# Optimization experiments

Hardware: AMD Instinct MI355X
Metric: run time of the kernel (lower is better)

## Reference

```python
import jax, jax.numpy as jnp
import numpy as np

N = 100000      # nodes
E = 3200000     # edges
G = 1024        # graphs in the batch
D_IN = 128      # input feature dim
H = 64          # hidden dim
BN_EPS = 1e-5


def _linear_init(key, fan_in, shape):
    bound = 1.0 / np.sqrt(fan_in)
    return jax.random.uniform(key, shape, jnp.float32, -bound, bound)


def setup_inputs() -> dict:
    key = jax.random.key(0)
    ks = jax.random.split(key, 16)
    x = jax.random.normal(ks[0], (N, D_IN), jnp.float32)
    edge_index = jax.random.randint(ks[1], (2, E), 0, N, dtype=jnp.int32)
    batch = jnp.sort(jax.random.randint(ks[2], (N,), 0, G, dtype=jnp.int32))
    inp = {"x": x, "edge_index": edge_index, "batch": batch}
    # layer 0 MLP: Linear(D_IN,H) -> ReLU -> BN(H) -> Linear(H,H) -> ReLU
    inp["W1_0"] = _linear_init(ks[3], D_IN, (D_IN, H))
    inp["b1_0"] = _linear_init(ks[4], D_IN, (H,))
    inp["g_0"] = jnp.ones((H,), jnp.float32)
    inp["be_0"] = jnp.zeros((H,), jnp.float32)
    inp["W2_0"] = _linear_init(ks[5], H, (H, H))
    inp["b2_0"] = _linear_init(ks[6], H, (H,))
    # layer 1 MLP: Linear(H,H) -> ReLU -> BN(H) -> Linear(H,H) -> ReLU
    inp["W1_1"] = _linear_init(ks[7], H, (H, H))
    inp["b1_1"] = _linear_init(ks[8], H, (H,))
    inp["g_1"] = jnp.ones((H,), jnp.float32)
    inp["be_1"] = jnp.zeros((H,), jnp.float32)
    inp["W2_1"] = _linear_init(ks[9], H, (H, H))
    inp["b2_1"] = _linear_init(ks[10], H, (H,))
    return inp


def _mlp(h, W1, b1, g, be, W2, b2):
    h = jnp.maximum(h @ W1 + b1, 0.0)
    mu = h.mean(axis=0)                      # BatchNorm1d (training: batch stats)
    var = h.var(axis=0)                      # biased variance, as torch normalizes
    h = g * (h - mu) * jax.lax.rsqrt(var + BN_EPS) + be
    return jnp.maximum(h @ W2 + b2, 0.0)


def _gin(h, src, dst, mlp_params):
    # GINConv, eps=0: out = mlp(x_i + sum_{j->i} x_j)
    agg = jax.ops.segment_sum(h[src], dst, num_segments=N)
    return _mlp(h + agg, *mlp_params)


def reference(x, edge_index, batch,
              W1_0, b1_0, g_0, be_0, W2_0, b2_0,
              W1_1, b1_1, g_1, be_1, W2_1, b2_1):
    src, dst = edge_index[0], edge_index[1]
    h = _gin(x, src, dst, (W1_0, b1_0, g_0, be_0, W2_0, b2_0))
    h = _gin(h, src, dst, (W1_1, b1_1, g_1, be_1, W2_1, b2_1))
    x_g = jax.ops.segment_sum(h, batch, num_segments=G)  # global add pooling
    return (x_g, h)
```

## Files before the change

### kernel.cpp

```cpp
#include <hip/hip_runtime.h>

static inline int cdiv_ll(long long a, long long b){ return (int)((a + b - 1) / b); }

#define EB_CHUNK 8192
#define NPB 256
#define MAXNB 512
#define CSR_LDS 10240

typedef short bf16x8 __attribute__((ext_vector_type(8)));
typedef float f32x4 __attribute__((ext_vector_type(4)));

__device__ __forceinline__ float bf2f(unsigned short h) {
  unsigned u = (unsigned)h << 16;
  return __uint_as_float(u);
}
__device__ __forceinline__ unsigned short f2bf(float f) {
  unsigned u = __float_as_uint(f);
  u += 0x7FFF + ((u >> 16) & 1);
  return (unsigned short)(u >> 16);
}

#define SWZ(row, byteoff) ((byteoff) ^ (((row) & 7) << 4))

template<int K, bool RELU>
__device__ __forceinline__ void stage_x_bf16(
    char* XlB, const float* __restrict__ X, long long rb, int M)
{
  for (int f = threadIdx.x; f < 16 * K; f += 256) {
    int r = f / (K / 4), c4 = (f % (K / 4)) * 4;
    float4 v = make_float4(0.f, 0.f, 0.f, 0.f);
    if (rb + r < M) {
      v = *reinterpret_cast<const float4*>(X + (rb + r) * K + c4);
      if (RELU) {
        v.x = fmaxf(v.x, 0.f); v.y = fmaxf(v.y, 0.f);
        v.z = fmaxf(v.z, 0.f); v.w = fmaxf(v.w, 0.f);
      }
    }
    ushort4 h; h.x = f2bf(v.x); h.y = f2bf(v.y); h.z = f2bf(v.z); h.w = f2bf(v.w);
    *reinterpret_cast<ushort4*>(XlB + r * (2 * K) + SWZ(r, c4 * 2)) = h;
  }
}

template<int K>
__device__ __forceinline__ void stage_wt_bf16(char* WTB, const float* __restrict__ W)
{
  for (int t = threadIdx.x; t < K * 32; t += 256) {
    int c = t & 63, kp = t >> 6;
    float w0 = W[(2 * kp) * 64 + c];
    float w1 = W[(2 * kp + 1) * 64 + c];
    ushort2 hh; hh.x = f2bf(w0); hh.y = f2bf(w1);
    *reinterpret_cast<ushort2*>(WTB + c * (2 * K) + SWZ(c, 4 * kp)) = hh;
  }
}

template<int K>
__device__ __forceinline__ void mfma_chain(
    f32x4* acc, const char* XlB, const char* WTB, int wv, int lr, int lg)
{
  const int rowb = 16 * wv + lr;
  #pragma unroll
  for (int kc = 0; kc < K / 32; ++kc) {
    const int kByte = kc * 64 + lg * 16;
    bf16x8 a = *reinterpret_cast<const bf16x8*>(XlB + rowb * (2 * K) + SWZ(rowb, kByte));
    #pragma unroll
    for (int ct = 0; ct < 4; ++ct) {
      int c = ct * 16 + lr;
      bf16x8 b = *reinterpret_cast<const bf16x8*>(WTB + c * (2 * K) + SWZ(c, kByte));
      acc[ct] = __builtin_amdgcn_mfma_f32_16x16x32_bf16(a, b, acc[ct], 0, 0, 0);
    }
  }
}

template<int K, bool IN_RELU, bool RELU_OUT, bool BIAS, bool OUT_BF16>
__global__ __launch_bounds__(256) void mfma_gemm(
    const float* __restrict__ X, const float* __restrict__ W,
    const float* __restrict__ bias, void* __restrict__ Yv, int M)
{
  __shared__ __align__(16) char XlB[64 * 2 * K];
  __shared__ __align__(16) char WTB[64 * 2 * K];
  const long long rb = (long long)blockIdx.x * 64;
  stage_x_bf16<K, IN_RELU>(XlB, X, rb, M);
  stage_wt_bf16<K>(WTB, W);
  __syncthreads();

  const int lane = threadIdx.x & 63, wv = threadIdx.x >> 6;
  const int lr = lane & 15, lg = lane >> 4;
  f32x4 acc[4] = {};
  mfma_chain<K>(acc, XlB, WTB, wv, lr, lg);

  #pragma unroll
  for (int ct = 0; ct < 4; ++ct) {
    const int c = ct * 16 + lr;
    const float bv = BIAS ? bias[c] : 0.0f;
    #pragma unroll
    for (int j = 0; j < 4; ++j) {
      long long row = rb + 16 * wv + lg * 4 + j;
      if (row < M) {
        float v = acc[ct][j] + bv;
        if (RELU_OUT) v = fmaxf(v, 0.f);
        if (OUT_BF16) ((unsigned short*)Yv)[row * 64 + c] = f2bf(v);
        else          ((float*)Yv)[row * 64 + c] = v;
      }
    }
  }
}

__global__ __launch_bounds__(256) void mfma_dual(
    const float* __restrict__ A, const float* __restrict__ Wa,
    const float* __restrict__ ba, const float* __restrict__ Wb,
    unsigned short* __restrict__ P, int M)
{
  __shared__ __align__(16) char XlB[64 * 128];
  __shared__ __align__(16) char WTaB[64 * 128];
  __shared__ __align__(16) char WTbB[64 * 128];
  __shared__ __align__(16) char Xl2B[64 * 128];
  const long long rb = (long long)blockIdx.x * 64;
  stage_x_bf16<64, true>(XlB, A, rb, M);
  stage_wt_bf16<64>(WTaB, Wa);
  stage_wt_bf16<64>(WTbB, Wb);
  __syncthreads();

  const int lane = threadIdx.x & 63, wv = threadIdx.x >> 6;
  const int lr = lane & 15, lg = lane >> 4;
  f32x4 acc[4] = {};
  mfma_chain<64>(acc, XlB, WTaB, wv, lr, lg);

  #pragma unroll
  for (int ct = 0; ct < 4; ++ct) {
    const int c = ct * 16 + lr;
    const float bv = ba[c];
    #pragma unroll
    for (int j = 0; j < 4; ++j) {
      int rloc = 16 * wv + lg * 4 + j;
      float v = fmaxf(acc[ct][j] + bv, 0.f);
      *reinterpret_cast<unsigned short*>(Xl2B + rloc * 128 + SWZ(rloc, c * 2)) = f2bf(v);
    }
  }
  __syncthreads();

  f32x4 ac2[4] = {};
  mfma_chain<64>(ac2, Xl2B, WTbB, wv, lr, lg);

  #pragma unroll
  for (int ct = 0; ct < 4; ++ct) {
    const int c = ct * 16 + lr;
    #pragma unroll
    for (int j = 0; j < 4; ++j) {
      long long row = rb + 16 * wv + lg * 4 + j;
      if (row < M) P[row * 64 + c] = f2bf(ac2[ct][j]);
    }
  }
}

__global__ __launch_bounds__(256) void part_hist(
    const int* __restrict__ dst, int* __restrict__ blockHist,
    int E, int NB, int nblocksB)
{
  __shared__ int hist[MAXNB];
  for (int i = threadIdx.x; i < NB; i += 256) hist[i] = 0;
  __syncthreads();
  int base = blockIdx.x * EB_CHUNK;
  int end = min(base + EB_CHUNK, E);
  for (int e = base + threadIdx.x; e < end; e += 256)
    atomicAdd(&hist[dst[e] >> 8], 1);
  __syncthreads();
  for (int i = threadIdx.x; i < NB; i += 256)
    blockHist[(long long)i * nblocksB + blockIdx.x] = hist[i];
}

__global__ __launch_bounds__(256) void scan_bucket_blocks(
    int* __restrict__ blockHist, int* __restrict__ bucketTotal, int nblocksB)
{
  int* row = blockHist + (long long)blockIdx.x * nblocksB;
  __shared__ int tsum[256];
  int v[4]; int local = 0;
  int i0 = threadIdx.x * 4;
  #pragma unroll
  for (int k = 0; k < 4; ++k) { int g = i0 + k; v[k] = (g < nblocksB) ? row[g] : 0; local += v[k]; }
  tsum[threadIdx.x] = local;
  __syncthreads();
  for (int off = 1; off < 256; off <<= 1) {
    int y = (threadIdx.x >= off) ? tsum[threadIdx.x - off] : 0;
    __syncthreads();
    tsum[threadIdx.x] += y;
    __syncthreads();
  }
  int pref = tsum[threadIdx.x] - local;
  #pragma unroll
  for (int k = 0; k < 4; ++k) { int g = i0 + k; if (g < nblocksB) { row[g] = pref; pref += v[k]; } }
  if (threadIdx.x == 255) bucketTotal[blockIdx.x] = tsum[255];
}

__global__ __launch_bounds__(512) void scan_buckets(
    const int* __restrict__ bucketTotal, int* __restrict__ bucketBase, int NB)
{
  __shared__ int tsum[512];
  int t = threadIdx.x;
  int v = (t < NB) ? bucketTotal[t] : 0;
  tsum[t] = v;
  __syncthreads();
  for (int off = 1; off < 512; off <<= 1) {
    int y = (t >= off) ? tsum[t - off] : 0;
    __syncthreads();
    tsum[t] += y;
    __syncthreads();
  }
  if (t < NB) bucketBase[t] = tsum[t] - v;
  if (t == NB - 1) bucketBase[NB] = tsum[t];
}

__global__ __launch_bounds__(256) void part_scatter(
    const int* __restrict__ src, const int* __restrict__ dst,
    const int* __restrict__ blockHist, const int* __restrict__ bucketBase,
    unsigned* __restrict__ ebuf, int E, int NB, int nblocksB)
{
  __shared__ int cursor[MAXNB];
  for (int i = threadIdx.x; i < NB; i += 256)
    cursor[i] = bucketBase[i] + blockHist[(long long)i * nblocksB + blockIdx.x];
  __syncthreads();
  int base = blockIdx.x * EB_CHUNK;
  int end = min(base + EB_CHUNK, E);
  for (int e = base + threadIdx.x; e < end; e += 256) {
    int s = src[e], d = dst[e];
    int p = atomicAdd(&cursor[d >> 8], 1);
    ebuf[p] = (unsigned)s | ((unsigned)(d & (NPB - 1)) << 24);
  }
}

__global__ __launch_bounds__(256) void bucket_csr(
    const unsigned* __restrict__ ebuf, const int* __restrict__ bucketBase,
    int* __restrict__ rowptr, int* __restrict__ col, int N, int NB)
{
  int b = blockIdx.x;
  int eb = bucketBase[b], ee = bucketBase[b + 1];
  int cnt = ee - eb;
  int nodeBase = b * NPB;
  __shared__ unsigned ebl[CSR_LDS];
  __shared__ int hist[NPB];
  __shared__ int tsum[NPB];
  __shared__ int cur[NPB];
  const bool fit = (cnt <= CSR_LDS);
  hist[threadIdx.x] = 0;
  if (fit) for (int i = threadIdx.x; i < cnt; i += 256) ebl[i] = ebuf[eb + i];
  __syncthreads();
  for (int i = threadIdx.x; i < cnt; i += 256)
    atomicAdd(&hist[(fit ? ebl[i] : ebuf[eb + i]) >> 24], 1);
  __syncthreads();
  int local = hist[threadIdx.x];
  tsum[threadIdx.x] = local;
  __syncthreads();
  for (int off = 1; off < 256; off <<= 1) {
    int y = (threadIdx.x >= off) ? tsum[threadIdx.x - off] : 0;
    __syncthreads();
    tsum[threadIdx.x] += y;
    __syncthreads();
  }
  int pref = tsum[threadIdx.x] - local;
  int node = nodeBase + threadIdx.x;
  if (node < N) rowptr[node] = eb + pref;
  if (b == NB - 1 && threadIdx.x == 0) rowptr[N] = ee;
  cur[threadIdx.x] = pref;
  __syncthreads();
  for (int i = threadIdx.x; i < cnt; i += 256) {
    unsigned w = fit ? ebl[i] : ebuf[eb + i];
    int l = (int)(w >> 24);
    int p = eb + atomicAdd(&cur[l], 1);
    col[p] = (int)(w & 0xFFFFFFu);
  }
}

__global__ __launch_bounds__(256) void gin_gather_bf16(
    const int* __restrict__ rowptr, const int* __restrict__ col,
    const unsigned short* __restrict__ P, const float* __restrict__ b1,
    float* __restrict__ A, float* __restrict__ stats, int N, int nodeStride)
{
  const int lane = threadIdx.x & 63;
  const int wv = threadIdx.x >> 6;
  const int q = lane >> 4;
  const int cl = lane & 15;
  float s[4] = {0.f, 0.f, 0.f, 0.f};
  float sq[4] = {0.f, 0.f, 0.f, 0.f};
  const float4 bb = *reinterpret_cast<const float4*>(b1 + 4 * cl);

  for (int node = blockIdx.x * 4 + wv; node < N; node += nodeStride) {
    const int beg = rowptr[node], end = rowptr[node + 1];
    float a0 = 0.f, a1 = 0.f, a2 = 0.f, a3 = 0.f;
    if (q == 1) {
      ushort4 h = *reinterpret_cast<const ushort4*>(P + (long long)node * 64 + 4 * cl);
      a0 = bf2f(h.x); a1 = bf2f(h.y); a2 = bf2f(h.z); a3 = bf2f(h.w);
    } else if (q == 2) {
      a0 = bb.x; a1 = bb.y; a2 = bb.z; a3 = bb.w;
    }
    int j = beg + q;
    for (; j + 12 < end; j += 16) {
      int rA = col[j], rB = col[j + 4], rC = col[j + 8], rD = col[j + 12];
      ushort4 hA = *reinterpret_cast<const ushort4*>(P + (long long)rA * 64 + 4 * cl);
      ushort4 hB = *reinterpret_cast<const ushort4*>(P + (long long)rB * 64 + 4 * cl);
      ushort4 hC = *reinterpret_cast<const ushort4*>(P + (long long)rC * 64 + 4 * cl);
      ushort4 hD = *reinterpret_cast<const ushort4*>(P + (long long)rD * 64 + 4 * cl);
      a0 += bf2f(hA.x); a1 += bf2f(hA.y); a2 += bf2f(hA.z); a3 += bf2f(hA.w);
      a0 += bf2f(hB.x); a1 += bf2f(hB.y); a2 += bf2f(hB.z); a3 += bf2f(hB.w);
      a0 += bf2f(hC.x); a1 += bf2f(hC.y); a2 += bf2f(hC.z); a3 += bf2f(hC.w);
      a0 += bf2f(hD.x); a1 += bf2f(hD.y); a2 += bf2f(hD.z); a3 += bf2f(hD.w);
    }
    for (; j < end; j += 4) {
      int rA = col[j];
      ushort4 hA = *reinterpret_cast<const ushort4*>(P + (long long)rA * 64 + 4 * cl);
      a0 += bf2f(hA.x); a1 += bf2f(hA.y); a2 += bf2f(hA.z); a3 += bf2f(hA.w);
    }
    a0 += __shfl_xor(a0, 16); a0 += __shfl_xor(a0, 32);
    a1 += __shfl_xor(a1, 16); a1 += __shfl_xor(a1, 32);
    a2 += __shfl_xor(a2, 16); a2 += __shfl_xor(a2, 32);
    a3 += __shfl_xor(a3, 16); a3 += __shfl_xor(a3, 32);
    if (q == 0) {
      *reinterpret_cast<float4*>(A + (long long)node * 64 + 4 * cl) =
          make_float4(a0, a1, a2, a3);
    } else if (q == 1) {
      float r0 = fmaxf(a0, 0.f), r1 = fmaxf(a1, 0.f);
      float r2 = fmaxf(a2, 0.f), r3 = fmaxf(a3, 0.f);
      s[0] += r0; s[1] += r1; s[2] += r2; s[3] += r3;
      sq[0] += r0 * r0; sq[1] += r1 * r1; sq[2] += r2 * r2; sq[3] += r3 * r3;
    }
  }

  __shared__ float st[4][16][8];
  if (q == 1) {
    st[wv][cl][0] = s[0]; st[wv][cl][1] = s[1]; st[wv][cl][2] = s[2]; st[wv][cl][3] = s[3];
    st[wv][cl][4] = sq[0]; st[wv][cl][5] = sq[1]; st[wv][cl][6] = sq[2]; st[wv][cl][7] = sq[3];
  }
  __syncthreads();
  if (threadIdx.x < 128) {
    int c = threadIdx.x;
    int colid = c & 63, part = c >> 6;
    int idx = (part ? 4 : 0) + (colid & 3);
    float v = st[0][colid >> 2][idx] + st[1][colid >> 2][idx]
            + st[2][colid >> 2][idx] + st[3][colid >> 2][idx];
    atomicAdd(&stats[c], v);
  }
}

__global__ void bn_fold(
    const float* __restrict__ stats, const float* __restrict__ g, const float* __restrict__ be,
    const float* __restrict__ W2, const float* __restrict__ b2,
    float* __restrict__ W2f, float* __restrict__ b2f, float invN)
{
  int j = threadIdx.x;
  __shared__ float sc[64], sh[64];
  float mu = stats[j] * invN;
  float var = stats[64 + j] * invN - mu * mu;
  float s = g[j] * rsqrtf(var + 1e-5f);
  sc[j] = s;
  sh[j] = be[j] - mu * s;
  __syncthreads();
  float acc = b2[j];
  for (int k = 0; k < 64; ++k) {
    float w = W2[k * 64 + j];
    W2f[k * 64 + j] = sc[k] * w;
    acc += sh[k] * w;
  }
  b2f[j] = acc;
}

__global__ __launch_bounds__(256) void pool_sorted(
    const float* __restrict__ Hf, const int* __restrict__ batch,
    float* __restrict__ out, int N, int G)
{
  int g = blockIdx.x * 4 + (threadIdx.x >> 6);
  int c = threadIdx.x & 63;
  if (g >= G) return;
  int lo = 0, hi = N;
  while (lo < hi) { int mid = (lo + hi) >> 1; if (batch[mid] < g) lo = mid + 1; else hi = mid; }
  int beg = lo;
  hi = N;
  while (lo < hi) { int mid = (lo + hi) >> 1; if (batch[mid] < g + 1) lo = mid + 1; else hi = mid; }
  int end = lo;
  float acc = 0.f;
  for (int r = beg; r < end; ++r) acc += Hf[(long long)r * 64 + c];
  out[(long long)g * 64 + c] = acc;
}

extern "C" void kernel_launch(void* const* d_in, const int* in_sizes, int n_in,
                              void* d_out, int out_size, void* d_ws, size_t ws_size,
                              hipStream_t stream) {
  const float* x      = (const float*)d_in[0];
  const int*   ei     = (const int*)d_in[1];
  const int*   batch  = (const int*)d_in[2];
  const float* W1_0 = (const float*)d_in[3];
  const float* b1_0 = (const float*)d_in[4];
  const float* g_0  = (const float*)d_in[5];
  const float* be_0 = (const float*)d_in[6];
  const float* W2_0 = (const float*)d_in[7];
  const float* b2_0 = (const float*)d_in[8];
  const float* W1_1 = (const float*)d_in[9];
  const float* b1_1 = (const float*)d_in[10];
  const float* g_1  = (const float*)d_in[11];
  const float* be_1 = (const float*)d_in[12];
  const float* W2_1 = (const float*)d_in[13];
  const float* b2_1 = (const float*)d_in[14];

  const int N = in_sizes[0] / 128;
  const int E = in_sizes[1] / 2;
  const int G = (out_size - N * 64) / 64;
  const int* srcI = ei;
  const int* dstI = ei + E;

  float* outG = (float*)d_out;
  float* outH = (float*)d_out + (long long)G * 64;

  const int NB = cdiv_ll(N, NPB);
  const int nblocksB = cdiv_ll(E, EB_CHUNK);

  char* w = (char*)d_ws;
  size_t r2 = (size_t)E * 4;
  if ((size_t)N * 64 * 2 > r2) r2 = (size_t)N * 64 * 2;
  unsigned* ebuf        = (unsigned*)w;
  unsigned short* Pbuf  = (unsigned short*)w;
  w += r2;
  int* col       = (int*)w; w += (size_t)E * 4;
  int* rowptr    = (int*)w; w += (size_t)(N + 1) * 4;
  int* blockHist = (int*)w; w += (size_t)NB * nblocksB * 4;
  int* bucketTotal = (int*)w; w += (size_t)NB * 4;
  int* bucketBase  = (int*)w; w += (size_t)(NB + 1) * 4;
  float* stats0 = (float*)w; w += 128 * 4;
  float* stats1 = (float*)w; w += 128 * 4;
  float* W2f0   = (float*)w; w += 64 * 64 * 4;
  float* b2f0   = (float*)w; w += 64 * 4;
  float* W2f1   = (float*)w; w += 64 * 64 * 4;
  float* b2f1   = (float*)w; w += 64 * 4;

  const int gemmGrid = cdiv_ll(N, 64);
  const int gatherGrid = 2048;

  hipMemsetAsync(stats0, 0, 256 * sizeof(float), stream);

  part_hist<<<nblocksB, 256, 0, stream>>>(dstI, blockHist, E, NB, nblocksB);
  scan_bucket_blocks<<<NB, 256, 0, stream>>>(blockHist, bucketTotal, nblocksB);
  scan_buckets<<<1, 512, 0, stream>>>(bucketTotal, bucketBase, NB);
  part_scatter<<<nblocksB, 256, 0, stream>>>(srcI, dstI, blockHist, bucketBase, ebuf, E, NB, nblocksB);
  bucket_csr<<<NB, 256, 0, stream>>>(ebuf, bucketBase, rowptr, col, N, NB);

  mfma_gemm<128, false, false, false, true><<<gemmGrid, 256, 0, stream>>>(x, W1_0, nullptr, Pbuf, N);
  gin_gather_bf16<<<gatherGrid, 256, 0, stream>>>(rowptr, col, Pbuf, b1_0, outH, stats0, N, gatherGrid * 4);
  bn_fold<<<1, 64, 0, stream>>>(stats0, g_0, be_0, W2_0, b2_0, W2f0, b2f0, 1.0f / N);
  mfma_dual<<<gemmGrid, 256, 0, stream>>>(outH, W2f0, b2f0, W1_1, Pbuf, N);

  gin_gather_bf16<<<gatherGrid, 256, 0, stream>>>(rowptr, col, Pbuf, b1_1, outH, stats1, N, gatherGrid * 4);
  bn_fold<<<1, 64, 0, stream>>>(stats1, g_1, be_1, W2_1, b2_1, W2f1, b2f1, 1.0f / N);
  mfma_gemm<64, true, true, true, false><<<gemmGrid, 256, 0, stream>>>(outH, W2f1, b2f1, outH, N);

  pool_sorted<<<cdiv_ll(G, 4), 256, 0, stream>>>(outH, batch, outG, N, G);
}
```

Measured before the change: 408.2 us.

## Split layer-0 projected features into 16-column panels and gather per panel

The first GEMM now writes its bf16 output as four column panels of 16 features each, laid out [panel][node][16], instead of row-major 64-wide rows. The layer-0 aggregation becomes four panel-gather launches, each reading 32-byte rows so that each panel (about 3.2 MB) fits in cache during the random neighbour gather. Each launch processes 8 edges per wavefront in parallel and reduces across lanes with shuffles. The cost is re-reading rowptr/col four times, more kernel launches, and smaller per-edge memory transactions.

```diff
diff --git a/kernel.cpp b/kernel.cpp
--- a/kernel.cpp
+++ b/kernel.cpp
@@ -71,7 +71,7 @@
   }
 }
 
-template<int K, bool IN_RELU, bool RELU_OUT, bool BIAS, bool OUT_BF16>
+template<int K, bool IN_RELU, bool RELU_OUT, bool BIAS, int OUT>
 __global__ __launch_bounds__(256) void mfma_gemm(
     const float* __restrict__ X, const float* __restrict__ W,
     const float* __restrict__ bias, void* __restrict__ Yv, int M)
@@ -98,8 +98,8 @@
       if (row < M) {
         float v = acc[ct][j] + bv;
         if (RELU_OUT) v = fmaxf(v, 0.f);
-        if (OUT_BF16) ((unsigned short*)Yv)[row * 64 + c] = f2bf(v);
-        else          ((float*)Yv)[row * 64 + c] = v;
+        if (OUT == 0) ((float*)Yv)[row * 64 + c] = v;
+        else ((unsigned short*)Yv)[(size_t)ct * M * 16 + row * 16 + lr] = f2bf(v);
       }
     }
   }
@@ -266,6 +266,60 @@
     int l = (int)(w >> 24);
     int p = eb + atomicAdd(&cur[l], 1);
     col[p] = (int)(w & 0xFFFFFFu);
+  }
+}
+
+__global__ __launch_bounds__(256) void gin_panel_gather(
+    const int* __restrict__ rowptr, const int* __restrict__ col,
+    const unsigned short* __restrict__ Pp, const float* __restrict__ b1,
+    float* __restrict__ A, float* __restrict__ stats, int N, int p, int nodeStride)
+{
+  const int lane = threadIdx.x & 63;
+  const int wv = threadIdx.x >> 6;
+  const int slot = lane >> 3;
+  const int sl = lane & 7;
+  const int c0 = p * 16 + 2 * sl;
+  const float bx = b1[c0], by = b1[c0 + 1];
+  float s0 = 0.f, s1 = 0.f, q0 = 0.f, q1 = 0.f;
+
+  for (int node = blockIdx.x * 4 + wv; node < N; node += nodeStride) {
+    const int beg = rowptr[node], end = rowptr[node + 1];
+    float a0 = 0.f, a1 = 0.f;
+    int j = beg + slot;
+    for (; j + 8 < end; j += 16) {
+      int rA = col[j], rB = col[j + 8];
+      ushort2 hA = *reinterpret_cast<const ushort2*>(Pp + (size_t)rA * 16 + 2 * sl);
+      ushort2 hB = *reinterpret_cast<const ushort2*>(Pp + (size_t)rB * 16 + 2 * sl);
+      a0 += bf2f(hA.x); a1 += bf2f(hA.y);
+      a0 += bf2f(hB.x); a1 += bf2f(hB.y);
+    }
+    if (j < end) {
+      int rA = col[j];
+      ushort2 hA = *reinterpret_cast<const ushort2*>(Pp + (size_t)rA * 16 + 2 * sl);
+      a0 += bf2f(hA.x); a1 += bf2f(hA.y);
+    }
+    a0 += __shfl_xor(a0, 8); a0 += __shfl_xor(a0, 16); a0 += __shfl_xor(a0, 32);
+    a1 += __shfl_xor(a1, 8); a1 += __shfl_xor(a1, 16); a1 += __shfl_xor(a1, 32);
+    if (slot == 0) {
+      ushort2 hs = *reinterpret_cast<const ushort2*>(Pp + (size_t)node * 16 + 2 * sl);
+      float v0 = a0 + bf2f(hs.x) + bx;
+      float v1 = a1 + bf2f(hs.y) + by;
+      *reinterpret_cast<float2*>(A + (size_t)node * 64 + c0) = make_float2(v0, v1);
+      float r0 = fmaxf(v0, 0.f), r1 = fmaxf(v1, 0.f);
+      s0 += r0; q0 += r0 * r0; s1 += r1; q1 += r1 * r1;
+    }
+  }
+
+  __shared__ float st[4][8][4];
+  if (slot == 0) {
+    st[wv][sl][0] = s0; st[wv][sl][1] = s1; st[wv][sl][2] = q0; st[wv][sl][3] = q1;
+  }
+  __syncthreads();
+  if (threadIdx.x < 32) {
+    int sl2 = threadIdx.x >> 2, f = threadIdx.x & 3;
+    float v = st[0][sl2][f] + st[1][sl2][f] + st[2][sl2][f] + st[3][sl2][f];
+    int c = p * 16 + 2 * sl2 + (f & 1);
+    atomicAdd(&stats[(f >= 2 ? 64 : 0) + c], v);
   }
 }
 
@@ -439,14 +493,16 @@
   part_scatter<<<nblocksB, 256, 0, stream>>>(srcI, dstI, blockHist, bucketBase, ebuf, E, NB, nblocksB);
   bucket_csr<<<NB, 256, 0, stream>>>(ebuf, bucketBase, rowptr, col, N, NB);
 
-  mfma_gemm<128, false, false, false, true><<<gemmGrid, 256, 0, stream>>>(x, W1_0, nullptr, Pbuf, N);
-  gin_gather_bf16<<<gatherGrid, 256, 0, stream>>>(rowptr, col, Pbuf, b1_0, outH, stats0, N, gatherGrid * 4);
+  mfma_gemm<128, false, false, false, 2><<<gemmGrid, 256, 0, stream>>>(x, W1_0, nullptr, Pbuf, N);
+  for (int p = 0; p < 4; ++p)
+    gin_panel_gather<<<gatherGrid, 256, 0, stream>>>(
+        rowptr, col, Pbuf + (size_t)p * N * 16, b1_0, outH, stats0, N, p, gatherGrid * 4);
   bn_fold<<<1, 64, 0, stream>>>(stats0, g_0, be_0, W2_0, b2_0, W2f0, b2f0, 1.0f / N);
   mfma_dual<<<gemmGrid, 256, 0, stream>>>(outH, W2f0, b2f0, W1_1, Pbuf, N);
 
   gin_gather_bf16<<<gatherGrid, 256, 0, stream>>>(rowptr, col, Pbuf, b1_1, outH, stats1, N, gatherGrid * 4);
   bn_fold<<<1, 64, 0, stream>>>(stats1, g_1, be_1, W2_1, b2_1, W2f1, b2f1, 1.0f / N);
-  mfma_gemm<64, true, true, true, false><<<gemmGrid, 256, 0, stream>>>(outH, W2f1, b2f1, outH, N);
+  mfma_gemm<64, true, true, true, 0><<<gemmGrid, 256, 0, stream>>>(outH, W2f1, b2f1, outH, N);
 
   pool_sorted<<<cdiv_ll(G, 4), 256, 0, stream>>>(outH, batch, outG, N, G);
 }
```

Measured after the change: 516.8 us. 1.27x slower.
